# Kernel tuning notes

Hardware: AMD Instinct MI355X
Metric: run time of the kernel (lower is better)

Reference implementation:

```python
import jax, jax.numpy as jnp
import numpy as np

EPS = 1e-08
N = 8192
IN_F = 128
OUT_F = 128


def setup_inputs() -> dict:
    key = jax.random.key(0)
    k1, k2, k3, k4, k5 = jax.random.split(key, 5)
    x = jax.random.normal(k1, (N, IN_F), dtype=jnp.float32)
    adj = jax.random.uniform(k2, (N, N), dtype=jnp.float32)
    noise = jax.random.uniform(k3, (N, N), dtype=jnp.float32)
    # xavier_uniform bound = sqrt(6/(in+out))
    bound = float(np.sqrt(6.0 / (IN_F + OUT_F)))
    weight = jax.random.uniform(k4, (IN_F, OUT_F), dtype=jnp.float32,
                                minval=-bound, maxval=bound)
    learnable_adj = jax.random.uniform(k5, (N, N), dtype=jnp.float32)
    return {"x": x, "adj": adj, "noise": noise, "weight": weight,
            "learnable_adj": learnable_adj}


def reference(x, adj, noise, weight, learnable_adj):
    # noise_adj = adj + learnable_adj + eps * rand_like(adj)
    noise_adj = adj + learnable_adj + EPS * noise
    # add self loops (== + eye(N))
    n = noise_adj.shape[0]
    looped_adj = noise_adj + jnp.eye(n, dtype=noise_adj.dtype)
    # symmetric degree normalization: diag(d^-1/2) @ A @ diag(d^-1/2),
    # expressed as row/col broadcast scaling (same math, O(n^2))
    degree = jnp.sum(looped_adj, axis=1)              # (N,)
    d_inv_sqrt = (degree + EPS) ** -0.5               # (N,)
    normalized_adj = looped_adj * d_inv_sqrt[:, None] * d_inv_sqrt[None, :]
    support = x @ weight                              # (N, out)
    out = normalized_adj @ support                    # (N, out)
    return out
```

## Files before the change

kernel.cpp:

```cpp
#include <hip/hip_runtime.h>
#include <hip/hip_bf16.h>
#include <cstddef>

#define NN 8192
#define FF 128
#define EPSF 1e-8f
#define KSPLIT 8

typedef __attribute__((ext_vector_type(8))) short short8_t;
typedef __attribute__((ext_vector_type(4))) float f32x4_t;

static __device__ __forceinline__ unsigned short f2bf(float f) {
    unsigned u = __builtin_bit_cast(unsigned, f);
    u = (u + 0x7FFFu + ((u >> 16) & 1u)) >> 16;
    return (unsigned short)u;
}
static __device__ __forceinline__ float bf2f(unsigned short h) {
    return __builtin_bit_cast(float, ((unsigned)h) << 16);
}

static __device__ __forceinline__ size_t lb2_idx(int row, int k) {
    return ((size_t)(row >> 4) * 256 + (k >> 5)) * 512
         + ((row & 15) * 4 + ((k >> 3) & 3)) * 8 + (k & 7);
}
static __device__ __forceinline__ size_t ss2_idx(int n, int k) {
    return ((size_t)(k >> 5) * 8 + (n >> 4)) * 512
         + ((n & 15) * 4 + ((k >> 3) & 3)) * 8 + (k & 7);
}

__global__ __launch_bounds__(256) void fuse_combine_kernel(
    const float* __restrict__ adj, const float* __restrict__ learn,
    unsigned short* __restrict__ Lb, float* __restrict__ degree)
{
    const int row = blockIdx.x >> 1;
    const int e0 = (blockIdx.x & 1) * 4096 + threadIdx.x * 8;
    const size_t base = (size_t)row * NN + e0;
    const f32x4_t a0 = __builtin_nontemporal_load((const f32x4_t*)(adj + base));
    const f32x4_t a1 = __builtin_nontemporal_load((const f32x4_t*)(adj + base + 4));
    const f32x4_t a2 = __builtin_nontemporal_load((const f32x4_t*)(adj + base + 2048));
    const f32x4_t a3 = __builtin_nontemporal_load((const f32x4_t*)(adj + base + 2052));
    const f32x4_t l0 = __builtin_nontemporal_load((const f32x4_t*)(learn + base));
    const f32x4_t l1 = __builtin_nontemporal_load((const f32x4_t*)(learn + base + 4));
    const f32x4_t l2 = __builtin_nontemporal_load((const f32x4_t*)(learn + base + 2048));
    const f32x4_t l3 = __builtin_nontemporal_load((const f32x4_t*)(learn + base + 2052));

    const f32x4_t v0 = a0 + l0, v1 = a1 + l1, v2 = a2 + l2, v3 = a3 + l3;
    short8_t p0, p1;
    p0[0] = (short)f2bf(v0.x); p0[1] = (short)f2bf(v0.y);
    p0[2] = (short)f2bf(v0.z); p0[3] = (short)f2bf(v0.w);
    p0[4] = (short)f2bf(v1.x); p0[5] = (short)f2bf(v1.y);
    p0[6] = (short)f2bf(v1.z); p0[7] = (short)f2bf(v1.w);
    p1[0] = (short)f2bf(v2.x); p1[1] = (short)f2bf(v2.y);
    p1[2] = (short)f2bf(v2.z); p1[3] = (short)f2bf(v2.w);
    p1[4] = (short)f2bf(v3.x); p1[5] = (short)f2bf(v3.y);
    p1[6] = (short)f2bf(v3.z); p1[7] = (short)f2bf(v3.w);
    *(short8_t*)(Lb + lb2_idx(row, e0)) = p0;
    *(short8_t*)(Lb + lb2_idx(row, e0 + 2048)) = p1;

    float acc = (v0.x + v0.y) + (v0.z + v0.w) + (v1.x + v1.y) + (v1.z + v1.w)
              + (v2.x + v2.y) + (v2.z + v2.w) + (v3.x + v3.y) + (v3.z + v3.w);
#pragma unroll
    for (int o = 32; o; o >>= 1) acc += __shfl_down(acc, o);
    __shared__ float red[4];
    if ((threadIdx.x & 63) == 0) red[threadIdx.x >> 6] = acc;
    __syncthreads();
    if (threadIdx.x == 0)
        atomicAdd(degree + row, red[0] + red[1] + red[2] + red[3]);
}

__global__ __launch_bounds__(256) void s_kernel(
    const float* __restrict__ degree, float* __restrict__ s)
{
    const int i = blockIdx.x * 256 + threadIdx.x;
    s[i] = rsqrtf(degree[i] + 1.0f + EPSF);
}

__global__ __launch_bounds__(256) void support_kernel(
    const float* __restrict__ x, const float* __restrict__ w,
    const float* __restrict__ s, unsigned short* __restrict__ ss2)
{
    __shared__ float Ws[128 * 128];
    __shared__ float Xs[32][128];
    for (int i = threadIdx.x; i < 128 * 128 / 4; i += 256)
        ((float4*)Ws)[i] = ((const float4*)w)[i];
    const int rbase = blockIdx.x * 32;
    for (int i = threadIdx.x; i < 32 * 128 / 4; i += 256)
        ((float4*)&Xs[0][0])[i] = ((const float4*)(x + (size_t)rbase * 128))[i];
    __syncthreads();

    const int c = threadIdx.x & 127;
    const int h = threadIdx.x >> 7;
    for (int r = h; r < 32; r += 2) {
        float acc = 0.f;
#pragma unroll 8
        for (int k = 0; k < 128; ++k) acc += Xs[r][k] * Ws[k * 128 + c];
        const int grow = rbase + r;
        ss2[ss2_idx(c, grow)] = f2bf(acc * s[grow]);
    }
}

template<bool ATOMIC>
__global__ __launch_bounds__(256) void spmm_bf16_kernel(
    const unsigned short* __restrict__ Lb,
    const unsigned short* __restrict__ ss2,
    const float* __restrict__ s, float* __restrict__ outp)
{
    const int ks   = blockIdx.y;
    const int i0   = blockIdx.x * 128;
    const int wave = threadIdx.x >> 6;
    const int lane = threadIdx.x & 63;
    const int m = lane & 15;
    const int b = lane >> 4;
    const int laneoff = (m * 4 + b) * 8;
    const int rb0 = (i0 >> 4) + wave * 2;
    const int kb0 = ks * (256 / KSPLIT);

    f32x4_t acc[2][8];
#pragma unroll
    for (int f = 0; f < 2; ++f)
#pragma unroll
        for (int t = 0; t < 8; ++t) acc[f][t] = (f32x4_t){0.f, 0.f, 0.f, 0.f};

    const unsigned short* a0p = Lb + (size_t)(rb0 + 0) * 256 * 512 + laneoff;
    const unsigned short* a1p = Lb + (size_t)(rb0 + 1) * 256 * 512 + laneoff;
    const unsigned short* bp  = ss2 + laneoff;

    for (int kb = kb0; kb < kb0 + 256 / KSPLIT; ++kb) {
        const unsigned short* bkb = bp + (size_t)kb * 4096;
        const short8_t b0 = *(const short8_t*)(bkb + 0 * 512);
        const short8_t b1 = *(const short8_t*)(bkb + 1 * 512);
        const short8_t b2 = *(const short8_t*)(bkb + 2 * 512);
        const short8_t b3 = *(const short8_t*)(bkb + 3 * 512);
        const short8_t b4 = *(const short8_t*)(bkb + 4 * 512);
        const short8_t b5 = *(const short8_t*)(bkb + 5 * 512);
        const short8_t b6 = *(const short8_t*)(bkb + 6 * 512);
        const short8_t b7 = *(const short8_t*)(bkb + 7 * 512);
        const short8_t af0 = *(const short8_t*)(a0p + (size_t)kb * 512);
        const short8_t af1 = *(const short8_t*)(a1p + (size_t)kb * 512);
        acc[0][0] = __builtin_amdgcn_mfma_f32_16x16x32_bf16(af0, b0, acc[0][0], 0, 0, 0);
        acc[1][0] = __builtin_amdgcn_mfma_f32_16x16x32_bf16(af1, b0, acc[1][0], 0, 0, 0);
        acc[0][1] = __builtin_amdgcn_mfma_f32_16x16x32_bf16(af0, b1, acc[0][1], 0, 0, 0);
        acc[1][1] = __builtin_amdgcn_mfma_f32_16x16x32_bf16(af1, b1, acc[1][1], 0, 0, 0);
        acc[0][2] = __builtin_amdgcn_mfma_f32_16x16x32_bf16(af0, b2, acc[0][2], 0, 0, 0);
        acc[1][2] = __builtin_amdgcn_mfma_f32_16x16x32_bf16(af1, b2, acc[1][2], 0, 0, 0);
        acc[0][3] = __builtin_amdgcn_mfma_f32_16x16x32_bf16(af0, b3, acc[0][3], 0, 0, 0);
        acc[1][3] = __builtin_amdgcn_mfma_f32_16x16x32_bf16(af1, b3, acc[1][3], 0, 0, 0);
        acc[0][4] = __builtin_amdgcn_mfma_f32_16x16x32_bf16(af0, b4, acc[0][4], 0, 0, 0);
        acc[1][4] = __builtin_amdgcn_mfma_f32_16x16x32_bf16(af1, b4, acc[1][4], 0, 0, 0);
        acc[0][5] = __builtin_amdgcn_mfma_f32_16x16x32_bf16(af0, b5, acc[0][5], 0, 0, 0);
        acc[1][5] = __builtin_amdgcn_mfma_f32_16x16x32_bf16(af1, b5, acc[1][5], 0, 0, 0);
        acc[0][6] = __builtin_amdgcn_mfma_f32_16x16x32_bf16(af0, b6, acc[0][6], 0, 0, 0);
        acc[1][6] = __builtin_amdgcn_mfma_f32_16x16x32_bf16(af1, b6, acc[1][6], 0, 0, 0);
        acc[0][7] = __builtin_amdgcn_mfma_f32_16x16x32_bf16(af0, b7, acc[0][7], 0, 0, 0);
        acc[1][7] = __builtin_amdgcn_mfma_f32_16x16x32_bf16(af1, b7, acc[1][7], 0, 0, 0);
    }

#pragma unroll
    for (int f = 0; f < 2; ++f) {
#pragma unroll
        for (int nt = 0; nt < 8; ++nt) {
            const int n = nt * 16 + m;
#pragma unroll
            for (int r = 0; r < 4; ++r) {
                const int ro = i0 + wave * 32 + f * 16 + 4 * b + r;
                float v = acc[f][nt][r];
                if (ATOMIC) {
                    if (ks == 0) v += bf2f(ss2[ss2_idx(n, ro)]);
                    atomicAdd(outp + (size_t)ro * FF + n, s[ro] * v);
                } else {
                    outp[(size_t)ks * NN * FF + (size_t)ro * FF + n] = v;
                }
            }
        }
    }
}

__global__ __launch_bounds__(256) void reduce_kernel(
    const float* __restrict__ part, const unsigned short* __restrict__ ss2,
    const float* __restrict__ s, float* __restrict__ out)
{
    const int idx4 = blockIdx.x * 256 + threadIdx.x;
    const int idx = idx4 * 4;
    const int gi = idx >> 7;
    const int cc = idx & 127;
    f32x4_t v = (f32x4_t){0.f, 0.f, 0.f, 0.f};
#pragma unroll
    for (int k = 0; k < KSPLIT; ++k)
        v += *(const f32x4_t*)(part + (size_t)k * NN * FF + idx);
    const float si = s[gi];
    float4 o;
    o.x = si * (v.x + bf2f(ss2[ss2_idx(cc + 0, gi)]));
    o.y = si * (v.y + bf2f(ss2[ss2_idx(cc + 1, gi)]));
    o.z = si * (v.z + bf2f(ss2[ss2_idx(cc + 2, gi)]));
    o.w = si * (v.w + bf2f(ss2[ss2_idx(cc + 3, gi)]));
    *(float4*)(out + idx) = o;
}

extern "C" void kernel_launch(void* const* d_in, const int* in_sizes, int n_in,
                              void* d_out, int out_size, void* d_ws, size_t ws_size,
                              hipStream_t stream) {
    const float* x     = (const float*)d_in[0];
    const float* adj   = (const float*)d_in[1];
    const float* w     = (const float*)d_in[3];
    const float* learn = (const float*)d_in[4];
    float* out = (float*)d_out;

    float* degree = (float*)d_ws;
    float* s      = degree + NN;
    unsigned short* ss2 = (unsigned short*)(s + NN);
    unsigned short* Lb  = ss2 + (size_t)FF * NN;
    float* part         = (float*)(Lb + (size_t)NN * NN);

    const size_t need_base = 2 * NN * 4 + (size_t)FF * NN * 2
                           + (size_t)NN * NN * 2;
    const size_t need_part = need_base + (size_t)KSPLIT * NN * FF * 4;

    hipMemsetAsync(degree, 0, NN * sizeof(float), stream);
    fuse_combine_kernel<<<NN * 2, 256, 0, stream>>>(adj, learn, Lb, degree);
    s_kernel<<<NN / 256, 256, 0, stream>>>(degree, s);
    support_kernel<<<NN / 32, 256, 0, stream>>>(x, w, s, ss2);

    if (ws_size >= need_part) {
        spmm_bf16_kernel<false><<<dim3(NN / 128, KSPLIT), 256, 0, stream>>>(
            Lb, ss2, s, part);
        reduce_kernel<<<NN * FF / 4 / 256, 256, 0, stream>>>(part, ss2, s, out);
    } else {
        hipMemsetAsync(d_out, 0, (size_t)NN * FF * sizeof(float), stream);
        spmm_bf16_kernel<true><<<dim3(NN / 128, KSPLIT), 256, 0, stream>>>(
            Lb, ss2, s, out);
    }
}
```

Measured before the change: 228.8 us.

## Fuse adjacency combine and bf16 conversion into the MFMA spmm loop

Removes the materialized bf16 combined adjacency buffer. A standalone degree kernel now computes the inverse sqrt degree directly, and the spmm kernel loads adj and learnable_adj in fp32, adds them and converts to bf16 in registers before the MFMAs. This drops the 128 MB bf16 write/read, the memset, the atomics and the separate s kernel. In exchange, the two fp32 N×N inputs are read twice from HBM, and the spmm's fp32 row loads are strided per lane.

```diff
diff --git a/kernel.cpp b/kernel.cpp
--- a/kernel.cpp
+++ b/kernel.cpp
@@ -11,68 +11,46 @@
 typedef __attribute__((ext_vector_type(4))) float f32x4_t;
 
 static __device__ __forceinline__ unsigned short f2bf(float f) {
-    unsigned u = __builtin_bit_cast(unsigned, f);
-    u = (u + 0x7FFFu + ((u >> 16) & 1u)) >> 16;
-    return (unsigned short)u;
+    __hip_bfloat16 h = __float2bfloat16(f);
+    return __builtin_bit_cast(unsigned short, h);
 }
 static __device__ __forceinline__ float bf2f(unsigned short h) {
     return __builtin_bit_cast(float, ((unsigned)h) << 16);
 }
-
-static __device__ __forceinline__ size_t lb2_idx(int row, int k) {
-    return ((size_t)(row >> 4) * 256 + (k >> 5)) * 512
-         + ((row & 15) * 4 + ((k >> 3) & 3)) * 8 + (k & 7);
-}
+static __device__ __forceinline__ f32x4_t ntl(const float* p) {
+    return __builtin_nontemporal_load((const f32x4_t*)p);
+}
+
 static __device__ __forceinline__ size_t ss2_idx(int n, int k) {
     return ((size_t)(k >> 5) * 8 + (n >> 4)) * 512
          + ((n & 15) * 4 + ((k >> 3) & 3)) * 8 + (k & 7);
 }
 
-__global__ __launch_bounds__(256) void fuse_combine_kernel(
+__global__ __launch_bounds__(256) void degree_kernel(
     const float* __restrict__ adj, const float* __restrict__ learn,
-    unsigned short* __restrict__ Lb, float* __restrict__ degree)
-{
-    const int row = blockIdx.x >> 1;
-    const int e0 = (blockIdx.x & 1) * 4096 + threadIdx.x * 8;
-    const size_t base = (size_t)row * NN + e0;
-    const f32x4_t a0 = __builtin_nontemporal_load((const f32x4_t*)(adj + base));
-    const f32x4_t a1 = __builtin_nontemporal_load((const f32x4_t*)(adj + base + 4));
-    const f32x4_t a2 = __builtin_nontemporal_load((const f32x4_t*)(adj + base + 2048));
-    const f32x4_t a3 = __builtin_nontemporal_load((const f32x4_t*)(adj + base + 2052));
-    const f32x4_t l0 = __builtin_nontemporal_load((const f32x4_t*)(learn + base));
-    const f32x4_t l1 = __builtin_nontemporal_load((const f32x4_t*)(learn + base + 4));
-    const f32x4_t l2 = __builtin_nontemporal_load((const f32x4_t*)(learn + base + 2048));
-    const f32x4_t l3 = __builtin_nontemporal_load((const f32x4_t*)(learn + base + 2052));
-
-    const f32x4_t v0 = a0 + l0, v1 = a1 + l1, v2 = a2 + l2, v3 = a3 + l3;
-    short8_t p0, p1;
-    p0[0] = (short)f2bf(v0.x); p0[1] = (short)f2bf(v0.y);
-    p0[2] = (short)f2bf(v0.z); p0[3] = (short)f2bf(v0.w);
-    p0[4] = (short)f2bf(v1.x); p0[5] = (short)f2bf(v1.y);
-    p0[6] = (short)f2bf(v1.z); p0[7] = (short)f2bf(v1.w);
-    p1[0] = (short)f2bf(v2.x); p1[1] = (short)f2bf(v2.y);
-    p1[2] = (short)f2bf(v2.z); p1[3] = (short)f2bf(v2.w);
-    p1[4] = (short)f2bf(v3.x); p1[5] = (short)f2bf(v3.y);
-    p1[6] = (short)f2bf(v3.z); p1[7] = (short)f2bf(v3.w);
-    *(short8_t*)(Lb + lb2_idx(row, e0)) = p0;
-    *(short8_t*)(Lb + lb2_idx(row, e0 + 2048)) = p1;
-
-    float acc = (v0.x + v0.y) + (v0.z + v0.w) + (v1.x + v1.y) + (v1.z + v1.w)
-              + (v2.x + v2.y) + (v2.z + v2.w) + (v3.x + v3.y) + (v3.z + v3.w);
+    float* __restrict__ s_out)
+{
+    const int row = blockIdx.x;
+    const size_t off = (size_t)row * NN;
+    const f32x4_t* a = (const f32x4_t*)(adj + off);
+    const f32x4_t* l = (const f32x4_t*)(learn + off);
+    float acc = 0.f;
+#pragma unroll
+    for (int it = 0; it < NN / 4 / 256; ++it) {
+        const f32x4_t av = a[threadIdx.x + it * 256];
+        const f32x4_t lv = l[threadIdx.x + it * 256];
+        acc += (av.x + av.y) + (av.z + av.w)
+             + (lv.x + lv.y) + (lv.z + lv.w);
+    }
 #pragma unroll
     for (int o = 32; o; o >>= 1) acc += __shfl_down(acc, o);
     __shared__ float red[4];
     if ((threadIdx.x & 63) == 0) red[threadIdx.x >> 6] = acc;
     __syncthreads();
-    if (threadIdx.x == 0)
-        atomicAdd(degree + row, red[0] + red[1] + red[2] + red[3]);
-}
-
-__global__ __launch_bounds__(256) void s_kernel(
-    const float* __restrict__ degree, float* __restrict__ s)
-{
-    const int i = blockIdx.x * 256 + threadIdx.x;
-    s[i] = rsqrtf(degree[i] + 1.0f + EPSF);
+    if (threadIdx.x == 0) {
+        const float d = red[0] + red[1] + red[2] + red[3] + 1.0f;
+        s_out[row] = rsqrtf(d + EPSF);
+    }
 }
 
 __global__ __launch_bounds__(256) void support_kernel(
@@ -100,8 +78,8 @@
 }
 
 template<bool ATOMIC>
-__global__ __launch_bounds__(256) void spmm_bf16_kernel(
-    const unsigned short* __restrict__ Lb,
+__global__ __launch_bounds__(256) void spmm_fused_kernel(
+    const float* __restrict__ adj, const float* __restrict__ learn,
     const unsigned short* __restrict__ ss2,
     const float* __restrict__ s, float* __restrict__ outp)
 {
@@ -112,20 +90,32 @@
     const int m = lane & 15;
     const int b = lane >> 4;
     const int laneoff = (m * 4 + b) * 8;
-    const int rb0 = (i0 >> 4) + wave * 2;
     const int kb0 = ks * (256 / KSPLIT);
 
+    const size_t r0off = (size_t)(i0 + wave * 32 + m) * NN;
+    const size_t r1off = r0off + (size_t)16 * NN;
+    const float* adj0 = adj + r0off;
+    const float* adj1 = adj + r1off;
+    const float* lrn0 = learn + r0off;
+    const float* lrn1 = learn + r1off;
+    const unsigned short* bp = ss2 + laneoff;
+
     f32x4_t acc[2][8];
 #pragma unroll
     for (int f = 0; f < 2; ++f)
 #pragma unroll
         for (int t = 0; t < 8; ++t) acc[f][t] = (f32x4_t){0.f, 0.f, 0.f, 0.f};
 
-    const unsigned short* a0p = Lb + (size_t)(rb0 + 0) * 256 * 512 + laneoff;
-    const unsigned short* a1p = Lb + (size_t)(rb0 + 1) * 256 * 512 + laneoff;
-    const unsigned short* bp  = ss2 + laneoff;
-
     for (int kb = kb0; kb < kb0 + 256 / KSPLIT; ++kb) {
+        const int kc = kb * 32 + 8 * b;
+        const f32x4_t A00 = ntl(adj0 + kc);
+        const f32x4_t A01 = ntl(adj0 + kc + 4);
+        const f32x4_t A10 = ntl(adj1 + kc);
+        const f32x4_t A11 = ntl(adj1 + kc + 4);
+        const f32x4_t L00 = ntl(lrn0 + kc);
+        const f32x4_t L01 = ntl(lrn0 + kc + 4);
+        const f32x4_t L10 = ntl(lrn1 + kc);
+        const f32x4_t L11 = ntl(lrn1 + kc + 4);
         const unsigned short* bkb = bp + (size_t)kb * 4096;
         const short8_t b0 = *(const short8_t*)(bkb + 0 * 512);
         const short8_t b1 = *(const short8_t*)(bkb + 1 * 512);
@@ -135,8 +125,17 @@
         const short8_t b5 = *(const short8_t*)(bkb + 5 * 512);
         const short8_t b6 = *(const short8_t*)(bkb + 6 * 512);
         const short8_t b7 = *(const short8_t*)(bkb + 7 * 512);
-        const short8_t af0 = *(const short8_t*)(a0p + (size_t)kb * 512);
-        const short8_t af1 = *(const short8_t*)(a1p + (size_t)kb * 512);
+        const f32x4_t v00 = A00 + L00, v01 = A01 + L01;
+        const f32x4_t v10 = A10 + L10, v11 = A11 + L11;
+        short8_t af0, af1;
+        af0[0] = (short)f2bf(v00.x); af0[1] = (short)f2bf(v00.y);
+        af0[2] = (short)f2bf(v00.z); af0[3] = (short)f2bf(v00.w);
+        af0[4] = (short)f2bf(v01.x); af0[5] = (short)f2bf(v01.y);
+        af0[6] = (short)f2bf(v01.z); af0[7] = (short)f2bf(v01.w);
+        af1[0] = (short)f2bf(v10.x); af1[1] = (short)f2bf(v10.y);
+        af1[2] = (short)f2bf(v10.z); af1[3] = (short)f2bf(v10.w);
+        af1[4] = (short)f2bf(v11.x); af1[5] = (short)f2bf(v11.y);
+        af1[6] = (short)f2bf(v11.z); af1[7] = (short)f2bf(v11.w);
         acc[0][0] = __builtin_amdgcn_mfma_f32_16x16x32_bf16(af0, b0, acc[0][0], 0, 0, 0);
         acc[1][0] = __builtin_amdgcn_mfma_f32_16x16x32_bf16(af1, b0, acc[1][0], 0, 0, 0);
         acc[0][1] = __builtin_amdgcn_mfma_f32_16x16x32_bf16(af0, b1, acc[0][1], 0, 0, 0);
@@ -205,28 +204,23 @@
     const float* learn = (const float*)d_in[4];
     float* out = (float*)d_out;
 
-    float* degree = (float*)d_ws;
-    float* s      = degree + NN;
+    float* s = (float*)d_ws;
     unsigned short* ss2 = (unsigned short*)(s + NN);
-    unsigned short* Lb  = ss2 + (size_t)FF * NN;
-    float* part         = (float*)(Lb + (size_t)NN * NN);
-
-    const size_t need_base = 2 * NN * 4 + (size_t)FF * NN * 2
-                           + (size_t)NN * NN * 2;
-    const size_t need_part = need_base + (size_t)KSPLIT * NN * FF * 4;
-
-    hipMemsetAsync(degree, 0, NN * sizeof(float), stream);
-    fuse_combine_kernel<<<NN * 2, 256, 0, stream>>>(adj, learn, Lb, degree);
-    s_kernel<<<NN / 256, 256, 0, stream>>>(degree, s);
+    float* part         = (float*)(ss2 + (size_t)FF * NN);
+
+    const size_t need_part = NN * 4 + (size_t)FF * NN * 2
+                           + (size_t)KSPLIT * NN * FF * 4;
+
+    degree_kernel<<<NN, 256, 0, stream>>>(adj, learn, s);
     support_kernel<<<NN / 32, 256, 0, stream>>>(x, w, s, ss2);
 
     if (ws_size >= need_part) {
-        spmm_bf16_kernel<false><<<dim3(NN / 128, KSPLIT), 256, 0, stream>>>(
-            Lb, ss2, s, part);
+        spmm_fused_kernel<false><<<dim3(NN / 128, KSPLIT), 256, 0, stream>>>(
+            adj, learn, ss2, s, part);
         reduce_kernel<<<NN * FF / 4 / 256, 256, 0, stream>>>(part, ss2, s, out);
     } else {
         hipMemsetAsync(d_out, 0, (size_t)NN * FF * sizeof(float), stream);
-        spmm_bf16_kernel<true><<<dim3(NN / 128, KSPLIT), 256, 0, stream>>>(
-            Lb, ss2, s, out);
-    }
-}
+        spmm_fused_kernel<true><<<dim3(NN / 128, KSPLIT), 256, 0, stream>>>(
+            adj, learn, ss2, s, out);
+    }
+}
```

New measurement: 265.0 us. 15.8% more time.
